# Kernel optimization log

Measured on AMD Instinct MI355X. Metric: run time of the kernel, lower is better.

## Reference

```python
import jax, jax.numpy as jnp
import numpy as np
import math

HEAD_SIZE = 64

def setup_inputs() -> dict:
    key = jax.random.key(0)
    k0, k1, k2, k3 = jax.random.split(key, 4)
    B, T, E, H = 4, 4096, 1024, HEAD_SIZE
    return {
        "x": jax.random.normal(k0, (B, T, E), dtype=jnp.float32),
        "Wq": jax.random.normal(k1, (E, H), dtype=jnp.float32) * (1.0 / math.sqrt(E)),
        "Wk": jax.random.normal(k2, (E, H), dtype=jnp.float32) * (1.0 / math.sqrt(E)),
        "Wv": jax.random.normal(k3, (E, H), dtype=jnp.float32) * (1.0 / math.sqrt(E)),
    }

def reference(x, Wq, Wk, Wv):
    # Single-head attention; faithful to source: softmax FIRST, then divide by sqrt(head_size)
    T = x.shape[-2]
    q = x @ Wq  # [B,T,H]
    k = x @ Wk
    v = x @ Wv
    scores = jnp.einsum('bth,bsh->bts', q, k)  # [B,T,T]
    # 'encoder' mask in this repo = lower-triangular (causal)
    causal = jnp.tril(jnp.ones((T, T), dtype=bool))
    scores = jnp.where(causal, scores, -jnp.inf)
    attn = jax.nn.softmax(scores, axis=-1) / jnp.sqrt(jnp.float32(q.shape[-1]))
    return jnp.einsum('bts,bsh->bth', attn, v)
```

## Files before the change

### kernel.cpp

```cpp
#include <hip/hip_runtime.h>
#include <math.h>

#define BB 4
#define TT 4096
#define EE 1024
#define HH 64

typedef __attribute__((ext_vector_type(8))) short bf16x8;
typedef __attribute__((ext_vector_type(4))) float f32x4;

#define MFMA16(a, b, c) __builtin_amdgcn_mfma_f32_16x16x32_bf16(a, b, c, 0, 0, 0)

__device__ __forceinline__ unsigned short f2bf_rne(float f) {
    unsigned u = __float_as_uint(f);
    unsigned r = u + 0x7fffu + ((u >> 16) & 1u);
    return (unsigned short)(r >> 16);
}
__device__ __forceinline__ float bf2f(unsigned short h) {
    return __uint_as_float(((unsigned)h) << 16);
}

__device__ __forceinline__ void async_copy16(const void* g, void* l) {
    __builtin_amdgcn_global_load_lds(
        (const __attribute__((address_space(1))) void*)g,
        (__attribute__((address_space(3))) void*)l, 16, 0, 0);
}
template<int N>
__device__ __forceinline__ void wait_vm() {
    __builtin_amdgcn_s_waitcnt(0x0f70 | (N & 15) | ((N >> 4) << 14));
}

__global__ __launch_bounds__(256) void wprep_kernel(
    const float* __restrict__ Wq, const float* __restrict__ Wk,
    const float* __restrict__ Wv,
    unsigned short* __restrict__ wt_hi, unsigned short* __restrict__ wt_lo)
{
    __shared__ float ts[64][65];
    const int which = blockIdx.x >> 4;
    const int e0 = (blockIdx.x & 15) * 64;
    const float* W = (which == 0) ? Wq : ((which == 1) ? Wk : Wv);
    const int t = threadIdx.x;
    const int h = t & 63;
    #pragma unroll
    for (int p = 0; p < 16; p++) {
        const int er = (t >> 6) + p * 4;
        ts[er][h] = W[(size_t)(e0 + er) * 64 + h];
    }
    __syncthreads();
    const int ew = t & 63;
    #pragma unroll
    for (int p = 0; p < 16; p++) {
        const int hh = (t >> 6) + p * 4;
        const float f = ts[ew][hh];
        const unsigned short hb = f2bf_rne(f);
        const unsigned short lb = f2bf_rne(f - bf2f(hb));
        const size_t o = (size_t)(which * 64 + hh) * 1024 + e0 + ew;
        wt_hi[o] = hb;
        wt_lo[o] = lb;
    }
}

__global__ __launch_bounds__(512) void proj_kernel(
    const float* __restrict__ x,
    const unsigned short* __restrict__ wt_hi, const unsigned short* __restrict__ wt_lo,
    unsigned short* __restrict__ qhi, unsigned short* __restrict__ qlo,
    unsigned short* __restrict__ khi, unsigned short* __restrict__ klo,
    unsigned short* __restrict__ vt)
{
    __shared__ __align__(16) unsigned char smem[98304];
    const int tid = threadIdx.x;
    const int w = tid >> 6, lane = tid & 63;
    const int quad = lane >> 4, li = lane & 15;
    const int tg = w & 3, eh = w >> 2;
    const int row0 = (int)blockIdx.x * 64;
    const int tok = row0 + tg * 16 + li;

    f32x4 acc[12];
    #pragma unroll
    for (int mt = 0; mt < 12; mt++) acc[mt] = (f32x4){0.f, 0.f, 0.f, 0.f};

    const float* xr = x + (size_t)tok * EE + eh * 512 + quad * 8;

    const int r_l = lane >> 3, sl = lane & 7;
    const int cg = sl ^ r_l;
    const unsigned short* mat = (cg < 4) ? wt_hi : wt_lo;
    const int ce = (cg & 3) * 8;
    const int sA = (quad ^ (li & 7)) * 8;
    const int sB = ((4 + quad) ^ (li & 7)) * 8;

    auto dma_step = [&](int e0, unsigned char* dstbase) {
        #pragma unroll
        for (int ii = 0; ii < 6; ii++) {
            const int i = w * 6 + ii;
            const int ehc = i / 24;
            const int within = i % 24;
            const int row = within * 8 + r_l;
            const unsigned short* src = mat + (size_t)row * EE + ehc * 512 + e0 + ce;
            async_copy16(src, dstbase + ehc * 24576 + within * 1024);
        }
    };

    dma_step(0, smem);
    float4 fc0 = *(const float4*)(xr + 0);
    float4 fc1 = *(const float4*)(xr + 4);
    float4 fn0, fn1;

    for (int s = 0; s < 16; s++) {
        const int e0 = s * 32;
        if (s < 15) {
            dma_step(e0 + 32, smem + ((s + 1) & 1) * 49152);
            fn0 = *(const float4*)(xr + e0 + 32);
            fn1 = *(const float4*)(xr + e0 + 36);
            wait_vm<8>();
        } else {
            wait_vm<0>();
        }
        __builtin_amdgcn_s_barrier();

        float fv[8] = {fc0.x, fc0.y, fc0.z, fc0.w, fc1.x, fc1.y, fc1.z, fc1.w};
        bf16x8 bh, bl;
        #pragma unroll
        for (int jj = 0; jj < 8; jj++) {
            unsigned short hb = f2bf_rne(fv[jj]);
            bh[jj] = (short)hb;
            bl[jj] = (short)f2bf_rne(fv[jj] - bf2f(hb));
        }
        const unsigned short* Wbase =
            (const unsigned short*)(smem + (s & 1) * 49152 + eh * 24576);
        #pragma unroll
        for (int mt = 0; mt < 12; mt++) {
            const unsigned short* rb = Wbase + (mt * 16 + li) * 64;
            bf16x8 Ah = *(const bf16x8*)(rb + sA);
            bf16x8 Al = *(const bf16x8*)(rb + sB);
            acc[mt] = MFMA16(Ah, bh, acc[mt]);
            acc[mt] = MFMA16(Ah, bl, acc[mt]);
            acc[mt] = MFMA16(Al, bh, acc[mt]);
        }
        __builtin_amdgcn_s_barrier();
        fc0 = fn0; fc1 = fn1;
    }

    float* Red = (float*)smem;
    if (eh == 1) {
        #pragma unroll
        for (int mt = 0; mt < 12; mt++)
            #pragma unroll
            for (int r = 0; r < 4; r++)
                Red[(size_t)(tg * 192 + mt * 16 + quad * 4 + r) * 17 + li] = acc[mt][r];
    }
    __syncthreads();
    if (eh == 0) {
        #pragma unroll
        for (int mt = 0; mt < 12; mt++)
            #pragma unroll
            for (int r = 0; r < 4; r++)
                acc[mt][r] += Red[(size_t)(tg * 192 + mt * 16 + quad * 4 + r) * 17 + li];
        const int bb = tok >> 12, tloc = tok & 4095;
        #pragma unroll
        for (int mt = 0; mt < 12; mt++) {
            if (mt < 8) {
                const int h = (mt & 3) * 16 + quad * 4;
                ushort4 hi4, lo4;
                unsigned short hb; float f;
                f = acc[mt][0]; hb = f2bf_rne(f); hi4.x = hb; lo4.x = f2bf_rne(f - bf2f(hb));
                f = acc[mt][1]; hb = f2bf_rne(f); hi4.y = hb; lo4.y = f2bf_rne(f - bf2f(hb));
                f = acc[mt][2]; hb = f2bf_rne(f); hi4.z = hb; lo4.z = f2bf_rne(f - bf2f(hb));
                f = acc[mt][3]; hb = f2bf_rne(f); hi4.w = hb; lo4.w = f2bf_rne(f - bf2f(hb));
                const size_t o = (size_t)tok * 64 + h;
                if (mt < 4) { *(ushort4*)(qhi + o) = hi4; *(ushort4*)(qlo + o) = lo4; }
                else        { *(ushort4*)(khi + o) = hi4; *(ushort4*)(klo + o) = lo4; }
            } else {
                const int hv = (mt - 8) * 16 + quad * 4;
                #pragma unroll
                for (int r = 0; r < 4; r++)
                    vt[((size_t)(bb * 64 + hv + r) << 12) + tloc] = f2bf_rne(acc[mt][r]);
            }
        }
    }
}

__global__ __launch_bounds__(256) void flash_kernel(
    const unsigned short* __restrict__ qhi, const unsigned short* __restrict__ qlo,
    const unsigned short* __restrict__ khi, const unsigned short* __restrict__ klo,
    const unsigned short* __restrict__ vt, float* __restrict__ out)
{
    __shared__ __align__(16) unsigned char smem[75776];
    const int tid = threadIdx.x;
    const int w = tid >> 6, lane = tid & 63;
    const int quad = lane >> 4, li = lane & 15;
    const int bx = (int)blockIdx.x;
    const int by = (int)blockIdx.y;
    const int hx = bx >> 1;
    const int g = (by < 2) ? ((bx & 1) ? hx : 127 - hx)
                           : ((bx & 1) ? 127 - hx : hx);
    const int b = by;
    const int q0 = g * 32;
    const int n_kt = g + 1;
    const int tok0 = q0 + li, tok1 = tok0 + 16;
    const float SM = 20.0f;

    const size_t qo0 = ((size_t)(b << 12) + tok0) * 64 + quad * 8;
    const size_t qo1 = qo0 + 16 * 64;
    const bf16x8 QhA0 = *(const bf16x8*)(qhi + qo0);
    const bf16x8 QhA1 = *(const bf16x8*)(qhi + qo0 + 32);
    const bf16x8 QlA0 = *(const bf16x8*)(qlo + qo0);
    const bf16x8 QlA1 = *(const bf16x8*)(qlo + qo0 + 32);
    const bf16x8 QhB0 = *(const bf16x8*)(qhi + qo1);
    const bf16x8 QhB1 = *(const bf16x8*)(qhi + qo1 + 32);
    const bf16x8 QlB0 = *(const bf16x8*)(qlo + qo1);
    const bf16x8 QlB1 = *(const bf16x8*)(qlo + qo1 + 32);

    const unsigned short* kb_hi = khi + ((size_t)b << 18);
    const unsigned short* kb_lo = klo + ((size_t)b << 18);
    const unsigned short* vtb   = vt  + ((size_t)b << 18) + (size_t)li * 4096 + quad * 8;

    unsigned char* kbase = smem + w * 16384;
    unsigned short* PsA = (unsigned short*)(smem + 65536 + w * 2560);
    unsigned short* PsB = PsA + 640;

    const int r_l4 = lane >> 4, s16 = lane & 15;
    const int slh0 = ((quad)      ^ li) * 8;
    const int slh1 = ((4 + quad)  ^ li) * 8;
    const int sll0 = ((8 + quad)  ^ li) * 8;
    const int sll1 = ((12 + quad) ^ li) * 8;

    auto dma_tile = [&](int k0, unsigned char* dst) {
        #pragma unroll
        for (int i = 0; i < 8; i++) {
            const int row = i * 4 + r_l4;
            const int c = s16 ^ (row & 15);
            const unsigned short* src = (c < 8)
                ? kb_hi + (size_t)(k0 + row) * 64 + c * 8
                : kb_lo + (size_t)(k0 + row) * 64 + (c - 8) * 8;
            async_copy16(src, dst + i * 1024);
        }
    };

    f32x4 accA[4], accB[4];
    #pragma unroll
    for (int mt = 0; mt < 4; mt++) {
        accA[mt] = (f32x4){0.f, 0.f, 0.f, 0.f};
        accB[mt] = (f32x4){0.f, 0.f, 0.f, 0.f};
    }
    float lA = 0.f, lB = 0.f;

    bf16x8 Vc[4], Vn[4];
    int bufp = 0;
    if (w < n_kt) {
        dma_tile(w * 32, kbase);
        #pragma unroll
        for (int hf = 0; hf < 4; hf++)
            Vc[hf] = *(const bf16x8*)(vtb + (size_t)hf * 65536 + w * 32);
    }

    for (int kt = w; kt < n_kt; kt += 4) {
        const int k0 = kt * 32;

        if (kt + 4 < n_kt) {
            dma_tile((kt + 4) * 32, kbase + (bufp ^ 1) * 8192);
            #pragma unroll
            for (int hf = 0; hf < 4; hf++)
                Vn[hf] = *(const bf16x8*)(vtb + (size_t)hf * 65536 + (kt + 4) * 32);
            wait_vm<12>();
        } else {
            wait_vm<0>();
        }
        const unsigned short* Kw = (const unsigned short*)(kbase + bufp * 8192);

        f32x4 sA[2], sB[2];
        #pragma unroll
        for (int jf = 0; jf < 2; jf++) {
            const unsigned short* rb = Kw + (jf * 16 + li) * 128;
            bf16x8 Kh0 = *(const bf16x8*)(rb + slh0);
            bf16x8 Kh1 = *(const bf16x8*)(rb + slh1);
            bf16x8 Kl0 = *(const bf16x8*)(rb + sll0);
            bf16x8 Kl1 = *(const bf16x8*)(rb + sll1);
            f32x4 a = (f32x4){0.f, 0.f, 0.f, 0.f};
            a = MFMA16(Kh0, QhA0, a);
            a = MFMA16(Kh1, QhA1, a);
            a = MFMA16(Kh0, QlA0, a);
            a = MFMA16(Kh1, QlA1, a);
            a = MFMA16(Kl0, QhA0, a);
            a = MFMA16(Kl1, QhA1, a);
            sA[jf] = a;
            f32x4 c2 = (f32x4){0.f, 0.f, 0.f, 0.f};
            c2 = MFMA16(Kh0, QhB0, c2);
            c2 = MFMA16(Kh1, QhB1, c2);
            c2 = MFMA16(Kh0, QlB0, c2);
            c2 = MFMA16(Kh1, QlB1, c2);
            c2 = MFMA16(Kl0, QhB0, c2);
            c2 = MFMA16(Kl1, QhB1, c2);
            sB[jf] = c2;
        }

        if (kt == n_kt - 1) {
            #pragma unroll
            for (int jf = 0; jf < 2; jf++)
                #pragma unroll
                for (int r = 0; r < 4; r++) {
                    const int j = k0 + jf * 16 + quad * 4 + r;
                    if (j > tok0) sA[jf][r] = -1e30f;
                    if (j > tok1) sB[jf][r] = -1e30f;
                }
        }

        #pragma unroll
        for (int jf = 0; jf < 2; jf++)
            #pragma unroll
            for (int r = 0; r < 4; r++) {
                sA[jf][r] = __expf(sA[jf][r] - SM); lA += sA[jf][r];
                sB[jf][r] = __expf(sB[jf][r] - SM); lB += sB[jf][r];
            }

        #pragma unroll
        for (int jf = 0; jf < 2; jf++) {
            ushort4 pa, pb;
            pa.x = f2bf_rne(sA[jf][0]); pa.y = f2bf_rne(sA[jf][1]);
            pa.z = f2bf_rne(sA[jf][2]); pa.w = f2bf_rne(sA[jf][3]);
            pb.x = f2bf_rne(sB[jf][0]); pb.y = f2bf_rne(sB[jf][1]);
            pb.z = f2bf_rne(sB[jf][2]); pb.w = f2bf_rne(sB[jf][3]);
            *(ushort4*)&PsA[li * 40 + jf * 16 + quad * 4] = pa;
            *(ushort4*)&PsB[li * 40 + jf * 16 + quad * 4] = pb;
        }
        const bf16x8 PA = *(const bf16x8*)&PsA[li * 40 + quad * 8];
        const bf16x8 PB = *(const bf16x8*)&PsB[li * 40 + quad * 8];

        #pragma unroll
        for (int hf = 0; hf < 4; hf++) {
            accA[hf] = MFMA16(Vc[hf], PA, accA[hf]);
            accB[hf] = MFMA16(Vc[hf], PB, accB[hf]);
        }
        #pragma unroll
        for (int hf = 0; hf < 4; hf++) Vc[hf] = Vn[hf];
        bufp ^= 1;
    }

    lA += __shfl_xor(lA, 16); lA += __shfl_xor(lA, 32);
    lB += __shfl_xor(lB, 16); lB += __shfl_xor(lB, 32);

    __syncthreads();
    float* Op = (float*)smem;
    float* Ml = (float*)(smem + 33792);
    #pragma unroll
    for (int mt = 0; mt < 4; mt++)
        #pragma unroll
        for (int r = 0; r < 4; r++) {
            Op[(size_t)w * 2112 + (mt * 16 + quad * 4 + r) * 33 + li]      = accA[mt][r];
            Op[(size_t)w * 2112 + (mt * 16 + quad * 4 + r) * 33 + li + 16] = accB[mt][r];
        }
    if (quad == 0) {
        Ml[w * 32 + li]      = lA;
        Ml[w * 32 + 16 + li] = lB;
    }
    __syncthreads();

    const int hc = (tid & 15) * 4;
    #pragma unroll
    for (int half = 0; half < 2; half++) {
        const int i = (tid >> 4) + half * 16;
        const float l = Ml[i] + Ml[32 + i] + Ml[64 + i] + Ml[96 + i];
        const float inv = 1.0f / (l * 8.0f);
        float4 o;
        o.x = (Op[(hc+0)*33+i] + Op[2112+(hc+0)*33+i] + Op[4224+(hc+0)*33+i] + Op[6336+(hc+0)*33+i]) * inv;
        o.y = (Op[(hc+1)*33+i] + Op[2112+(hc+1)*33+i] + Op[4224+(hc+1)*33+i] + Op[6336+(hc+1)*33+i]) * inv;
        o.z = (Op[(hc+2)*33+i] + Op[2112+(hc+2)*33+i] + Op[4224+(hc+2)*33+i] + Op[6336+(hc+2)*33+i]) * inv;
        o.w = (Op[(hc+3)*33+i] + Op[2112+(hc+3)*33+i] + Op[4224+(hc+3)*33+i] + Op[6336+(hc+3)*33+i]) * inv;
        *(float4*)(out + ((size_t)(b << 12) + q0 + i) * 64 + hc) = o;
    }
}

extern "C" void kernel_launch(void* const* d_in, const int* in_sizes, int n_in,
                              void* d_out, int out_size, void* d_ws, size_t ws_size,
                              hipStream_t stream)
{
    const float* x  = (const float*)d_in[0];
    const float* Wq = (const float*)d_in[1];
    const float* Wk = (const float*)d_in[2];
    const float* Wv = (const float*)d_in[3];
    float* out = (float*)d_out;

    const size_t n_tok = (size_t)BB * TT * HH;
    unsigned short* qhi = (unsigned short*)d_ws;
    unsigned short* qlo = qhi + n_tok;
    unsigned short* khi = qlo + n_tok;
    unsigned short* klo = khi + n_tok;
    unsigned short* vt  = klo + n_tok;
    unsigned short* wt_hi = vt + n_tok;
    unsigned short* wt_lo = wt_hi + 192 * 1024;

    wprep_kernel<<<48, 256, 0, stream>>>(Wq, Wk, Wv, wt_hi, wt_lo);
    proj_kernel<<<(BB * TT) / 64, 512, 0, stream>>>(x, wt_hi, wt_lo,
                                                    qhi, qlo, khi, klo, vt);
    flash_kernel<<<dim3(128, BB), 256, 0, stream>>>(qhi, qlo, khi, klo, vt, out);
}
```

Baseline: 169.7 us.

## Pair causal query tiles per block with 8 waves and triple-buffer projection loads

The flash kernel now launches 64x4 blocks of 512 threads. Each block processes two query tiles in sequence, g and 127-g, so every block does a balanced amount of causal work, and eight waves split the key tiles instead of four. The projection kernel moves from double to triple buffering of weight tiles and x loads, with a deeper prefetch distance. In exchange, shared memory use grows to about 148 KB per block, which limits occupancy to one block per CU, and the flash kernel adds an extra sequential phase per block.

```diff
diff --git a/kernel.cpp b/kernel.cpp
--- a/kernel.cpp
+++ b/kernel.cpp
@@ -67,7 +67,7 @@
     unsigned short* __restrict__ khi, unsigned short* __restrict__ klo,
     unsigned short* __restrict__ vt)
 {
-    __shared__ __align__(16) unsigned char smem[98304];
+    __shared__ __align__(16) unsigned char smem[147456];
     const int tid = threadIdx.x;
     const int w = tid >> 6, lane = tid & 63;
     const int quad = lane >> 4, li = lane & 15;
@@ -103,14 +103,19 @@
     dma_step(0, smem);
     float4 fc0 = *(const float4*)(xr + 0);
     float4 fc1 = *(const float4*)(xr + 4);
-    float4 fn0, fn1;
+    dma_step(32, smem + 49152);
+    float4 fn0 = *(const float4*)(xr + 32);
+    float4 fn1 = *(const float4*)(xr + 36);
+    float4 ff0, ff1;
 
     for (int s = 0; s < 16; s++) {
         const int e0 = s * 32;
-        if (s < 15) {
-            dma_step(e0 + 32, smem + ((s + 1) & 1) * 49152);
-            fn0 = *(const float4*)(xr + e0 + 32);
-            fn1 = *(const float4*)(xr + e0 + 36);
+        if (s + 2 < 16) {
+            dma_step(e0 + 64, smem + ((s + 2) % 3) * 49152);
+            ff0 = *(const float4*)(xr + e0 + 64);
+            ff1 = *(const float4*)(xr + e0 + 68);
+            wait_vm<16>();
+        } else if (s + 1 < 16) {
             wait_vm<8>();
         } else {
             wait_vm<0>();
@@ -126,7 +131,7 @@
             bl[jj] = (short)f2bf_rne(fv[jj] - bf2f(hb));
         }
         const unsigned short* Wbase =
-            (const unsigned short*)(smem + (s & 1) * 49152 + eh * 24576);
+            (const unsigned short*)(smem + (s % 3) * 49152 + eh * 24576);
         #pragma unroll
         for (int mt = 0; mt < 12; mt++) {
             const unsigned short* rb = Wbase + (mt * 16 + li) * 64;
@@ -137,7 +142,7 @@
             acc[mt] = MFMA16(Al, bh, acc[mt]);
         }
         __builtin_amdgcn_s_barrier();
-        fc0 = fn0; fc1 = fn1;
+        fc0 = fn0; fc1 = fn1; fn0 = ff0; fn1 = ff1;
     }
 
     float* Red = (float*)smem;
@@ -179,44 +184,28 @@
     }
 }
 
-__global__ __launch_bounds__(256) void flash_kernel(
+__global__ __launch_bounds__(512) void flash_kernel(
     const unsigned short* __restrict__ qhi, const unsigned short* __restrict__ qlo,
     const unsigned short* __restrict__ khi, const unsigned short* __restrict__ klo,
     const unsigned short* __restrict__ vt, float* __restrict__ out)
 {
-    __shared__ __align__(16) unsigned char smem[75776];
+    __shared__ __align__(16) unsigned char smem[151552];
     const int tid = threadIdx.x;
     const int w = tid >> 6, lane = tid & 63;
     const int quad = lane >> 4, li = lane & 15;
     const int bx = (int)blockIdx.x;
-    const int by = (int)blockIdx.y;
-    const int hx = bx >> 1;
-    const int g = (by < 2) ? ((bx & 1) ? hx : 127 - hx)
-                           : ((bx & 1) ? 127 - hx : hx);
-    const int b = by;
-    const int q0 = g * 32;
-    const int n_kt = g + 1;
-    const int tok0 = q0 + li, tok1 = tok0 + 16;
+    const int b = (int)blockIdx.y;
     const float SM = 20.0f;
-
-    const size_t qo0 = ((size_t)(b << 12) + tok0) * 64 + quad * 8;
-    const size_t qo1 = qo0 + 16 * 64;
-    const bf16x8 QhA0 = *(const bf16x8*)(qhi + qo0);
-    const bf16x8 QhA1 = *(const bf16x8*)(qhi + qo0 + 32);
-    const bf16x8 QlA0 = *(const bf16x8*)(qlo + qo0);
-    const bf16x8 QlA1 = *(const bf16x8*)(qlo + qo0 + 32);
-    const bf16x8 QhB0 = *(const bf16x8*)(qhi + qo1);
-    const bf16x8 QhB1 = *(const bf16x8*)(qhi + qo1 + 32);
-    const bf16x8 QlB0 = *(const bf16x8*)(qlo + qo1);
-    const bf16x8 QlB1 = *(const bf16x8*)(qlo + qo1 + 32);
 
     const unsigned short* kb_hi = khi + ((size_t)b << 18);
     const unsigned short* kb_lo = klo + ((size_t)b << 18);
     const unsigned short* vtb   = vt  + ((size_t)b << 18) + (size_t)li * 4096 + quad * 8;
 
     unsigned char* kbase = smem + w * 16384;
-    unsigned short* PsA = (unsigned short*)(smem + 65536 + w * 2560);
+    unsigned short* PsA = (unsigned short*)(smem + 131072 + w * 2560);
     unsigned short* PsB = PsA + 640;
+    float* Op = (float*)smem;
+    float* Ml = (float*)(smem + 67584);
 
     const int r_l4 = lane >> 4, s16 = lane & 15;
     const int slh0 = ((quad)      ^ li) * 8;
@@ -236,136 +225,158 @@
         }
     };
 
-    f32x4 accA[4], accB[4];
-    #pragma unroll
-    for (int mt = 0; mt < 4; mt++) {
-        accA[mt] = (f32x4){0.f, 0.f, 0.f, 0.f};
-        accB[mt] = (f32x4){0.f, 0.f, 0.f, 0.f};
-    }
-    float lA = 0.f, lB = 0.f;
-
-    bf16x8 Vc[4], Vn[4];
-    int bufp = 0;
-    if (w < n_kt) {
-        dma_tile(w * 32, kbase);
-        #pragma unroll
-        for (int hf = 0; hf < 4; hf++)
-            Vc[hf] = *(const bf16x8*)(vtb + (size_t)hf * 65536 + w * 32);
-    }
-
-    for (int kt = w; kt < n_kt; kt += 4) {
-        const int k0 = kt * 32;
-
-        if (kt + 4 < n_kt) {
-            dma_tile((kt + 4) * 32, kbase + (bufp ^ 1) * 8192);
+    #pragma unroll 1
+    for (int phase = 0; phase < 2; phase++) {
+        const int g = phase ? (127 - bx) : bx;
+        const int q0 = g * 32;
+        const int n_kt = g + 1;
+        const int tok0 = q0 + li, tok1 = tok0 + 16;
+
+        const size_t qo0 = ((size_t)(b << 12) + tok0) * 64 + quad * 8;
+        const size_t qo1 = qo0 + 16 * 64;
+        const bf16x8 QhA0 = *(const bf16x8*)(qhi + qo0);
+        const bf16x8 QhA1 = *(const bf16x8*)(qhi + qo0 + 32);
+        const bf16x8 QlA0 = *(const bf16x8*)(qlo + qo0);
+        const bf16x8 QlA1 = *(const bf16x8*)(qlo + qo0 + 32);
+        const bf16x8 QhB0 = *(const bf16x8*)(qhi + qo1);
+        const bf16x8 QhB1 = *(const bf16x8*)(qhi + qo1 + 32);
+        const bf16x8 QlB0 = *(const bf16x8*)(qlo + qo1);
+        const bf16x8 QlB1 = *(const bf16x8*)(qlo + qo1 + 32);
+
+        f32x4 accA[4], accB[4];
+        #pragma unroll
+        for (int mt = 0; mt < 4; mt++) {
+            accA[mt] = (f32x4){0.f, 0.f, 0.f, 0.f};
+            accB[mt] = (f32x4){0.f, 0.f, 0.f, 0.f};
+        }
+        float lA = 0.f, lB = 0.f;
+
+        bf16x8 Vc[4], Vn[4];
+        int bufp = 0;
+        if (w < n_kt) {
+            dma_tile(w * 32, kbase);
             #pragma unroll
             for (int hf = 0; hf < 4; hf++)
-                Vn[hf] = *(const bf16x8*)(vtb + (size_t)hf * 65536 + (kt + 4) * 32);
-            wait_vm<12>();
-        } else {
-            wait_vm<0>();
-        }
-        const unsigned short* Kw = (const unsigned short*)(kbase + bufp * 8192);
-
-        f32x4 sA[2], sB[2];
-        #pragma unroll
-        for (int jf = 0; jf < 2; jf++) {
-            const unsigned short* rb = Kw + (jf * 16 + li) * 128;
-            bf16x8 Kh0 = *(const bf16x8*)(rb + slh0);
-            bf16x8 Kh1 = *(const bf16x8*)(rb + slh1);
-            bf16x8 Kl0 = *(const bf16x8*)(rb + sll0);
-            bf16x8 Kl1 = *(const bf16x8*)(rb + sll1);
-            f32x4 a = (f32x4){0.f, 0.f, 0.f, 0.f};
-            a = MFMA16(Kh0, QhA0, a);
-            a = MFMA16(Kh1, QhA1, a);
-            a = MFMA16(Kh0, QlA0, a);
-            a = MFMA16(Kh1, QlA1, a);
-            a = MFMA16(Kl0, QhA0, a);
-            a = MFMA16(Kl1, QhA1, a);
-            sA[jf] = a;
-            f32x4 c2 = (f32x4){0.f, 0.f, 0.f, 0.f};
-            c2 = MFMA16(Kh0, QhB0, c2);
-            c2 = MFMA16(Kh1, QhB1, c2);
-            c2 = MFMA16(Kh0, QlB0, c2);
-            c2 = MFMA16(Kh1, QlB1, c2);
-            c2 = MFMA16(Kl0, QhB0, c2);
-            c2 = MFMA16(Kl1, QhB1, c2);
-            sB[jf] = c2;
-        }
-
-        if (kt == n_kt - 1) {
+                Vc[hf] = *(const bf16x8*)(vtb + (size_t)hf * 65536 + w * 32);
+        }
+
+        for (int kt = w; kt < n_kt; kt += 8) {
+            const int k0 = kt * 32;
+
+            if (kt + 8 < n_kt) {
+                dma_tile((kt + 8) * 32, kbase + (bufp ^ 1) * 8192);
+                #pragma unroll
+                for (int hf = 0; hf < 4; hf++)
+                    Vn[hf] = *(const bf16x8*)(vtb + (size_t)hf * 65536 + (kt + 8) * 32);
+                wait_vm<12>();
+            } else {
+                wait_vm<0>();
+            }
+            const unsigned short* Kw = (const unsigned short*)(kbase + bufp * 8192);
+
+            f32x4 sA[2], sB[2];
+            #pragma unroll
+            for (int jf = 0; jf < 2; jf++) {
+                const unsigned short* rb = Kw + (jf * 16 + li) * 128;
+                bf16x8 Kh0 = *(const bf16x8*)(rb + slh0);
+                bf16x8 Kh1 = *(const bf16x8*)(rb + slh1);
+                bf16x8 Kl0 = *(const bf16x8*)(rb + sll0);
+                bf16x8 Kl1 = *(const bf16x8*)(rb + sll1);
+                f32x4 a = (f32x4){0.f, 0.f, 0.f, 0.f};
+                a = MFMA16(Kh0, QhA0, a);
+                a = MFMA16(Kh1, QhA1, a);
+                a = MFMA16(Kh0, QlA0, a);
+                a = MFMA16(Kh1, QlA1, a);
+                a = MFMA16(Kl0, QhA0, a);
+                a = MFMA16(Kl1, QhA1, a);
+                sA[jf] = a;
+                f32x4 c2 = (f32x4){0.f, 0.f, 0.f, 0.f};
+                c2 = MFMA16(Kh0, QhB0, c2);
+                c2 = MFMA16(Kh1, QhB1, c2);
+                c2 = MFMA16(Kh0, QlB0, c2);
+                c2 = MFMA16(Kh1, QlB1, c2);
+                c2 = MFMA16(Kl0, QhB0, c2);
+                c2 = MFMA16(Kl1, QhB1, c2);
+                sB[jf] = c2;
+            }
+
+            if (kt == n_kt - 1) {
+                #pragma unroll
+                for (int jf = 0; jf < 2; jf++)
+                    #pragma unroll
+                    for (int r = 0; r < 4; r++) {
+                        const int j = k0 + jf * 16 + quad * 4 + r;
+                        if (j > tok0) sA[jf][r] = -1e30f;
+                        if (j > tok1) sB[jf][r] = -1e30f;
+                    }
+            }
+
             #pragma unroll
             for (int jf = 0; jf < 2; jf++)
                 #pragma unroll
                 for (int r = 0; r < 4; r++) {
-                    const int j = k0 + jf * 16 + quad * 4 + r;
-                    if (j > tok0) sA[jf][r] = -1e30f;
-                    if (j > tok1) sB[jf][r] = -1e30f;
+                    sA[jf][r] = __expf(sA[jf][r] - SM); lA += sA[jf][r];
+                    sB[jf][r] = __expf(sB[jf][r] - SM); lB += sB[jf][r];
                 }
-        }
-
-        #pragma unroll
-        for (int jf = 0; jf < 2; jf++)
+
+            #pragma unroll
+            for (int jf = 0; jf < 2; jf++) {
+                ushort4 pa, pb;
+                pa.x = f2bf_rne(sA[jf][0]); pa.y = f2bf_rne(sA[jf][1]);
+                pa.z = f2bf_rne(sA[jf][2]); pa.w = f2bf_rne(sA[jf][3]);
+                pb.x = f2bf_rne(sB[jf][0]); pb.y = f2bf_rne(sB[jf][1]);
+                pb.z = f2bf_rne(sB[jf][2]); pb.w = f2bf_rne(sB[jf][3]);
+                *(ushort4*)&PsA[li * 40 + jf * 16 + quad * 4] = pa;
+                *(ushort4*)&PsB[li * 40 + jf * 16 + quad * 4] = pb;
+            }
+            const bf16x8 PA = *(const bf16x8*)&PsA[li * 40 + quad * 8];
+            const bf16x8 PB = *(const bf16x8*)&PsB[li * 40 + quad * 8];
+
+            #pragma unroll
+            for (int hf = 0; hf < 4; hf++) {
+                accA[hf] = MFMA16(Vc[hf], PA, accA[hf]);
+                accB[hf] = MFMA16(Vc[hf], PB, accB[hf]);
+            }
+            #pragma unroll
+            for (int hf = 0; hf < 4; hf++) Vc[hf] = Vn[hf];
+            bufp ^= 1;
+        }
+
+        lA += __shfl_xor(lA, 16); lA += __shfl_xor(lA, 32);
+        lB += __shfl_xor(lB, 16); lB += __shfl_xor(lB, 32);
+
+        __syncthreads();
+        #pragma unroll
+        for (int mt = 0; mt < 4; mt++)
             #pragma unroll
             for (int r = 0; r < 4; r++) {
-                sA[jf][r] = __expf(sA[jf][r] - SM); lA += sA[jf][r];
-                sB[jf][r] = __expf(sB[jf][r] - SM); lB += sB[jf][r];
-            }
-
-        #pragma unroll
-        for (int jf = 0; jf < 2; jf++) {
-            ushort4 pa, pb;
-            pa.x = f2bf_rne(sA[jf][0]); pa.y = f2bf_rne(sA[jf][1]);
-            pa.z = f2bf_rne(sA[jf][2]); pa.w = f2bf_rne(sA[jf][3]);
-            pb.x = f2bf_rne(sB[jf][0]); pb.y = f2bf_rne(sB[jf][1]);
-            pb.z = f2bf_rne(sB[jf][2]); pb.w = f2bf_rne(sB[jf][3]);
-            *(ushort4*)&PsA[li * 40 + jf * 16 + quad * 4] = pa;
-            *(ushort4*)&PsB[li * 40 + jf * 16 + quad * 4] = pb;
-        }
-        const bf16x8 PA = *(const bf16x8*)&PsA[li * 40 + quad * 8];
-        const bf16x8 PB = *(const bf16x8*)&PsB[li * 40 + quad * 8];
-
-        #pragma unroll
-        for (int hf = 0; hf < 4; hf++) {
-            accA[hf] = MFMA16(Vc[hf], PA, accA[hf]);
-            accB[hf] = MFMA16(Vc[hf], PB, accB[hf]);
-        }
-        #pragma unroll
-        for (int hf = 0; hf < 4; hf++) Vc[hf] = Vn[hf];
-        bufp ^= 1;
-    }
-
-    lA += __shfl_xor(lA, 16); lA += __shfl_xor(lA, 32);
-    lB += __shfl_xor(lB, 16); lB += __shfl_xor(lB, 32);
-
-    __syncthreads();
-    float* Op = (float*)smem;
-    float* Ml = (float*)(smem + 33792);
-    #pragma unroll
-    for (int mt = 0; mt < 4; mt++)
-        #pragma unroll
-        for (int r = 0; r < 4; r++) {
-            Op[(size_t)w * 2112 + (mt * 16 + quad * 4 + r) * 33 + li]      = accA[mt][r];
-            Op[(size_t)w * 2112 + (mt * 16 + quad * 4 + r) * 33 + li + 16] = accB[mt][r];
-        }
-    if (quad == 0) {
-        Ml[w * 32 + li]      = lA;
-        Ml[w * 32 + 16 + li] = lB;
-    }
-    __syncthreads();
-
-    const int hc = (tid & 15) * 4;
-    #pragma unroll
-    for (int half = 0; half < 2; half++) {
-        const int i = (tid >> 4) + half * 16;
-        const float l = Ml[i] + Ml[32 + i] + Ml[64 + i] + Ml[96 + i];
+                Op[(size_t)w * 2112 + (mt * 16 + quad * 4 + r) * 33 + li]      = accA[mt][r];
+                Op[(size_t)w * 2112 + (mt * 16 + quad * 4 + r) * 33 + li + 16] = accB[mt][r];
+            }
+        if (quad == 0) {
+            Ml[w * 32 + li]      = lA;
+            Ml[w * 32 + 16 + li] = lB;
+        }
+        __syncthreads();
+
+        const int i  = tid >> 4;
+        const int hc = (tid & 15) * 4;
+        float l = 0.f;
+        #pragma unroll
+        for (int ww = 0; ww < 8; ww++) l += Ml[ww * 32 + i];
         const float inv = 1.0f / (l * 8.0f);
-        float4 o;
-        o.x = (Op[(hc+0)*33+i] + Op[2112+(hc+0)*33+i] + Op[4224+(hc+0)*33+i] + Op[6336+(hc+0)*33+i]) * inv;
-        o.y = (Op[(hc+1)*33+i] + Op[2112+(hc+1)*33+i] + Op[4224+(hc+1)*33+i] + Op[6336+(hc+1)*33+i]) * inv;
-        o.z = (Op[(hc+2)*33+i] + Op[2112+(hc+2)*33+i] + Op[4224+(hc+2)*33+i] + Op[6336+(hc+2)*33+i]) * inv;
-        o.w = (Op[(hc+3)*33+i] + Op[2112+(hc+3)*33+i] + Op[4224+(hc+3)*33+i] + Op[6336+(hc+3)*33+i]) * inv;
+        float4 o = {0.f, 0.f, 0.f, 0.f};
+        #pragma unroll
+        for (int ww = 0; ww < 8; ww++) {
+            const float* base = Op + (size_t)ww * 2112;
+            o.x += base[(hc + 0) * 33 + i];
+            o.y += base[(hc + 1) * 33 + i];
+            o.z += base[(hc + 2) * 33 + i];
+            o.w += base[(hc + 3) * 33 + i];
+        }
+        o.x *= inv; o.y *= inv; o.z *= inv; o.w *= inv;
         *(float4*)(out + ((size_t)(b << 12) + q0 + i) * 64 + hc) = o;
+        __syncthreads();
     }
 }
 
@@ -391,5 +402,5 @@
     wprep_kernel<<<48, 256, 0, stream>>>(Wq, Wk, Wv, wt_hi, wt_lo);
     proj_kernel<<<(BB * TT) / 64, 512, 0, stream>>>(x, wt_hi, wt_lo,
                                                     qhi, qlo, khi, klo, vt);
-    flash_kernel<<<dim3(128, BB), 256, 0, stream>>>(qhi, qlo, khi, klo, vt, out);
-}
+    flash_kernel<<<dim3(64, BB), 512, 0, stream>>>(qhi, qlo, khi, klo, vt, out);
+}
```

Measured after the change: 162.5 us. 4.2% less time.
